# Optimization experiments

Hardware: AMD Instinct MI355X
Metric: run time of the kernel (lower is better)

Reference implementation:

```python
import jax, jax.numpy as jnp
from jax import lax
import numpy as np

BATCH = 524288
SEQ_LEN = 64


def setup_inputs() -> dict:
    key = jax.random.key(0)
    ka, kb = jax.random.split(key)
    a = jax.random.randint(ka, (BATCH, SEQ_LEN), 0, 10).astype(jnp.float32)
    b = jax.random.randint(kb, (BATCH, SEQ_LEN), 0, 10).astype(jnp.float32)
    # RNNCell params as hardcoded in Adder._initialize_weights
    weight_ih = jnp.array([[1.0, 1.0]], dtype=jnp.float32)   # (hidden=1, input=2)
    weight_hh = jnp.array([[1.0]], dtype=jnp.float32)        # (1, 1)
    bias_ih = jnp.zeros((1,), dtype=jnp.float32)
    bias_hh = jnp.zeros((1,), dtype=jnp.float32)
    return {"a": a, "b": b, "weight_ih": weight_ih, "weight_hh": weight_hh,
            "bias_ih": bias_ih, "bias_hh": bias_hh}


def reference(a, b, weight_ih, weight_hh, bias_ih, bias_hh):
    # a, b: (B, S) base-10 digits; carry h: (B, 1) hidden state.
    # Process digits from least significant (rightmost) to most significant.
    xs = jnp.stack([a, b], axis=-1)            # (B, S, 2)
    xs = jnp.flip(xs, axis=1)                  # reversed digit order
    xs = jnp.swapaxes(xs, 0, 1)                # (S, B, 2) for scan

    def step(h, x):
        # RNNCell with relu: u = relu(x @ W_ih^T + b_ih + h @ W_hh^T + b_hh)
        u = jax.nn.relu(x @ weight_ih.T + bias_ih + h @ weight_hh.T + bias_hh)  # (B,1)
        carry = jax.nn.relu(u - 9.0) - jax.nn.relu(u - 10.0)                    # (B,1)
        s = x[:, 0] + x[:, 1] + h[:, 0]                                         # (B,)
        digit = s - 10.0 * carry[:, 0]                                          # (B,)
        return carry, digit

    h0 = jnp.zeros((a.shape[0], 1), dtype=a.dtype)
    _, digits_rev = lax.scan(step, h0, xs)     # (S, B), least-significant first
    digits = jnp.flip(digits_rev, axis=0).T    # (B, S), original order
    return digits
```

## Files before the change

### kernel.cpp

```cpp
#include <hip/hip_runtime.h>


__global__ __launch_bounds__(256) void adder_kernel(
    const float4* __restrict__ a,
    const float4* __restrict__ b,
    float4* __restrict__ out,
    long long n_rows)
{
    const int lane = (int)(threadIdx.x & 63);
    const int k    = lane >> 4;
    const int blk  = lane & 15;
    const int pos  = 15 - blk;

    const long long wave_id     = (long long)blockIdx.x * 4 + (threadIdx.x >> 6);
    const long long wave_stride = (long long)gridDim.x * 4;
    const long long n_wave_work = (n_rows + 3) >> 2;

    for (long long w = wave_id; w < n_wave_work; w += wave_stride) {
        const long long row = w * 4 + k;
        const bool ok = row < n_rows;
        const long long v4 = (ok ? row : 0) * 16 + blk;

        const float4 av = a[v4];
        const float4 bv = b[v4];
        const float s0 = av.x + bv.x;
        const float s1 = av.y + bv.y;
        const float s2 = av.z + bv.z;
        const float s3 = av.w + bv.w;

        float gc = (s3 >= 10.0f) ? 1.0f : 0.0f;
        gc = (s2 + gc >= 10.0f) ? 1.0f : 0.0f;
        gc = (s1 + gc >= 10.0f) ? 1.0f : 0.0f;
        gc = (s0 + gc >= 10.0f) ? 1.0f : 0.0f;
        const bool Gb = (gc != 0.0f);
        const bool Pb = (s0 == 9.0f) && (s1 == 9.0f) &&
                        (s2 == 9.0f) && (s3 == 9.0f);

        const unsigned long long g_mask = __ballot(Gb);
        const unsigned long long p_mask = __ballot(Pb);
        unsigned int g16 = (unsigned int)(g_mask >> (k * 16)) & 0xFFFFu;
        unsigned int p16 = (unsigned int)(p_mask >> (k * 16)) & 0xFFFFu;
        g16 = __brev(g16) >> 16;
        p16 = __brev(p16) >> 16;
        const unsigned int pg  = p16 | g16;
        const unsigned int c16 = (pg + g16) ^ pg ^ g16;
        const float cin = (float)((c16 >> pos) & 1u);

        const float u3 = s3 + cin; const float c3 = (u3 >= 10.0f) ? 1.0f : 0.0f;
        const float u2 = s2 + c3;  const float c2 = (u2 >= 10.0f) ? 1.0f : 0.0f;
        const float u1 = s1 + c2;  const float c1 = (u1 >= 10.0f) ? 1.0f : 0.0f;
        const float u0 = s0 + c1;  const float c0 = (u0 >= 10.0f) ? 1.0f : 0.0f;

        float4 dv;
        dv.x = u0 - 10.0f * c0;
        dv.y = u1 - 10.0f * c1;
        dv.z = u2 - 10.0f * c2;
        dv.w = u3 - 10.0f * c3;
        if (ok) out[v4] = dv;
    }
}

extern "C" void kernel_launch(void* const* d_in, const int* in_sizes, int n_in,
                              void* d_out, int out_size, void* d_ws, size_t ws_size,
                              hipStream_t stream) {
    const float4* a = (const float4*)d_in[0];
    const float4* b = (const float4*)d_in[1];
    float4* out = (float4*)d_out;

    const long long n_rows  = (long long)in_sizes[0] / 64;
    const long long n_waves = (n_rows + 3) / 4;
    long long blocks = (n_waves + 3) / 4;
    if (blocks > 2048) blocks = 2048;
    adder_kernel<<<(int)blocks, 256, 0, stream>>>(a, b, out, n_rows);
}
```

Before: 318.3 us.

## Batch four tile loads per wave and drop the persistent grid-stride loop

```diff
diff --git a/kernel.cpp b/kernel.cpp
--- a/kernel.cpp
+++ b/kernel.cpp
@@ -1,62 +1,77 @@
 #include <hip/hip_runtime.h>
 
+
+__device__ __forceinline__ float4 add_tile(const float4 av, const float4 bv,
+                                           const int k, const int pos) {
+    const float s0 = av.x + bv.x;
+    const float s1 = av.y + bv.y;
+    const float s2 = av.z + bv.z;
+    const float s3 = av.w + bv.w;
+
+    float gc = (s3 >= 10.0f) ? 1.0f : 0.0f;
+    gc = (s2 + gc >= 10.0f) ? 1.0f : 0.0f;
+    gc = (s1 + gc >= 10.0f) ? 1.0f : 0.0f;
+    gc = (s0 + gc >= 10.0f) ? 1.0f : 0.0f;
+    const bool Gb = (gc != 0.0f);
+    const bool Pb = (s0 == 9.0f) & (s1 == 9.0f) & (s2 == 9.0f) & (s3 == 9.0f);
+
+    const unsigned long long g_mask = __ballot(Gb);
+    const unsigned long long p_mask = __ballot(Pb);
+    unsigned int g16 = (unsigned int)(g_mask >> (k * 16)) & 0xFFFFu;
+    unsigned int p16 = (unsigned int)(p_mask >> (k * 16)) & 0xFFFFu;
+    g16 = __brev(g16) >> 16;
+    p16 = __brev(p16) >> 16;
+    const unsigned int pg  = p16 | g16;
+    const unsigned int c16 = (pg + g16) ^ pg ^ g16;
+    const float cin = (float)((c16 >> pos) & 1u);
+
+    const float u3 = s3 + cin; const float c3 = (u3 >= 10.0f) ? 1.0f : 0.0f;
+    const float u2 = s2 + c3;  const float c2 = (u2 >= 10.0f) ? 1.0f : 0.0f;
+    const float u1 = s1 + c2;  const float c1 = (u1 >= 10.0f) ? 1.0f : 0.0f;
+    const float u0 = s0 + c1;  const float c0 = (u0 >= 10.0f) ? 1.0f : 0.0f;
+
+    float4 dv;
+    dv.x = u0 - 10.0f * c0;
+    dv.y = u1 - 10.0f * c1;
+    dv.z = u2 - 10.0f * c2;
+    dv.w = u3 - 10.0f * c3;
+    return dv;
+}
 
 __global__ __launch_bounds__(256) void adder_kernel(
     const float4* __restrict__ a,
     const float4* __restrict__ b,
     float4* __restrict__ out,
-    long long n_rows)
+    long long n_tiles)
 {
     const int lane = (int)(threadIdx.x & 63);
     const int k    = lane >> 4;
-    const int blk  = lane & 15;
-    const int pos  = 15 - blk;
+    const int pos  = 15 - (lane & 15);
 
-    const long long wave_id     = (long long)blockIdx.x * 4 + (threadIdx.x >> 6);
-    const long long wave_stride = (long long)gridDim.x * 4;
-    const long long n_wave_work = (n_rows + 3) >> 2;
+    const long long wave_id = (long long)blockIdx.x * 4 + (threadIdx.x >> 6);
+    const long long t0 = wave_id * 4;
+    if (t0 >= n_tiles) return;
 
-    for (long long w = wave_id; w < n_wave_work; w += wave_stride) {
-        const long long row = w * 4 + k;
-        const bool ok = row < n_rows;
-        const long long v4 = (ok ? row : 0) * 16 + blk;
+    if (t0 + 4 <= n_tiles) {
+        const long long i0 = t0 * 64 + lane;
+        const float4 a0 = a[i0];
+        const float4 b0 = b[i0];
+        const float4 a1 = a[i0 + 64];
+        const float4 b1 = b[i0 + 64];
+        const float4 a2 = a[i0 + 128];
+        const float4 b2 = b[i0 + 128];
+        const float4 a3 = a[i0 + 192];
+        const float4 b3 = b[i0 + 192];
 
-        const float4 av = a[v4];
-        const float4 bv = b[v4];
-        const float s0 = av.x + bv.x;
-        const float s1 = av.y + bv.y;
-        const float s2 = av.z + bv.z;
-        const float s3 = av.w + bv.w;
-
-        float gc = (s3 >= 10.0f) ? 1.0f : 0.0f;
-        gc = (s2 + gc >= 10.0f) ? 1.0f : 0.0f;
-        gc = (s1 + gc >= 10.0f) ? 1.0f : 0.0f;
-        gc = (s0 + gc >= 10.0f) ? 1.0f : 0.0f;
-        const bool Gb = (gc != 0.0f);
-        const bool Pb = (s0 == 9.0f) && (s1 == 9.0f) &&
-                        (s2 == 9.0f) && (s3 == 9.0f);
-
-        const unsigned long long g_mask = __ballot(Gb);
-        const unsigned long long p_mask = __ballot(Pb);
-        unsigned int g16 = (unsigned int)(g_mask >> (k * 16)) & 0xFFFFu;
-        unsigned int p16 = (unsigned int)(p_mask >> (k * 16)) & 0xFFFFu;
-        g16 = __brev(g16) >> 16;
-        p16 = __brev(p16) >> 16;
-        const unsigned int pg  = p16 | g16;
-        const unsigned int c16 = (pg + g16) ^ pg ^ g16;
-        const float cin = (float)((c16 >> pos) & 1u);
-
-        const float u3 = s3 + cin; const float c3 = (u3 >= 10.0f) ? 1.0f : 0.0f;
-        const float u2 = s2 + c3;  const float c2 = (u2 >= 10.0f) ? 1.0f : 0.0f;
-        const float u1 = s1 + c2;  const float c1 = (u1 >= 10.0f) ? 1.0f : 0.0f;
-        const float u0 = s0 + c1;  const float c0 = (u0 >= 10.0f) ? 1.0f : 0.0f;
-
-        float4 dv;
-        dv.x = u0 - 10.0f * c0;
-        dv.y = u1 - 10.0f * c1;
-        dv.z = u2 - 10.0f * c2;
-        dv.w = u3 - 10.0f * c3;
-        if (ok) out[v4] = dv;
+        out[i0]       = add_tile(a0, b0, k, pos);
+        out[i0 + 64]  = add_tile(a1, b1, k, pos);
+        out[i0 + 128] = add_tile(a2, b2, k, pos);
+        out[i0 + 192] = add_tile(a3, b3, k, pos);
+    } else {
+        for (long long t = t0; t < n_tiles; ++t) {
+            const long long i = t * 64 + lane;
+            out[i] = add_tile(a[i], b[i], k, pos);
+        }
     }
 }
 
@@ -68,8 +83,8 @@
     float4* out = (float4*)d_out;
 
     const long long n_rows  = (long long)in_sizes[0] / 64;
-    const long long n_waves = (n_rows + 3) / 4;
-    long long blocks = (n_waves + 3) / 4;
-    if (blocks > 2048) blocks = 2048;
-    adder_kernel<<<(int)blocks, 256, 0, stream>>>(a, b, out, n_rows);
+    const long long n_tiles = (n_rows + 3) / 4;
+    const long long n_waves = (n_tiles + 3) / 4;
+    const long long blocks  = (n_waves + 3) / 4;
+    adder_kernel<<<(int)blocks, 256, 0, stream>>>(a, b, out, n_tiles);
 }
```

After: 309.8 us. -2.7%, faster.
